# Kernel optimization log

Hardware: AMD Instinct MI355X
Metric: run time of the kernel (lower is better)

## Reference

```python
import jax, jax.numpy as jnp
import numpy as np

N = 100000   # nodes
E = 800000   # edges
IN = 256     # input feature dim
H = 4        # heads per layer
D = 32       # per-head hidden dim (num_hidden)
SLOPE = 0.2  # leaky_relu negative slope


def setup_inputs() -> dict:
    key = jax.random.key(0)
    ks = jax.random.split(key, 8)
    s = 0.1  # weight scale for numerical stability
    x = jax.random.normal(ks[0], (N, IN), jnp.float32)
    edge_index = jax.random.randint(ks[1], (2, E), 0, N, dtype=jnp.int32)
    W0 = jax.random.normal(ks[2], (IN, H * D), jnp.float32) * s
    al0 = jax.random.normal(ks[3], (H, D), jnp.float32) * s
    ar0 = jax.random.normal(ks[4], (H, D), jnp.float32) * s
    W1 = jax.random.normal(ks[5], (H * D, H * D), jnp.float32) * s
    al1 = jax.random.normal(ks[6], (H, D), jnp.float32) * s
    ar1 = jax.random.normal(ks[7], (H, D), jnp.float32) * s
    return {"x": x, "edge_index": edge_index, "W0": W0, "al0": al0,
            "ar0": ar0, "W1": W1, "al1": al1, "ar1": ar1}


def _gat_layer(h, W, al, ar, src, dst, residual):
    """One GATConv: project, edge attention, dst-wise softmax, scatter-agg."""
    n = h.shape[0]
    feat = (h @ W).reshape(n, H, D)              # [N,H,D]
    el = jnp.einsum('nhd,hd->nh', feat, al)      # [N,H]
    er = jnp.einsum('nhd,hd->nh', feat, ar)      # [N,H]
    e = jax.nn.leaky_relu(el[src] + er[dst], SLOPE)   # raw scores [E,H]
    # edge softmax grouped by destination node (numerically stable)
    emax = jax.ops.segment_max(e, dst, num_segments=n)   # [N,H]
    eexp = jnp.exp(e - emax[dst])                          # [E,H]
    denom = jax.ops.segment_sum(eexp, dst, num_segments=n)  # [N,H]
    a = eexp / denom[dst]                                  # attention [E,H]
    msg = feat[src] * a[:, :, None]                        # [E,H,D]
    rst = jax.ops.segment_sum(msg, dst, num_segments=n)    # [N,H,D]
    if residual:
        rst = rst + h.reshape(n, H, D)  # identity residual (dims match)
    rst = jax.nn.elu(rst)               # activation
    return rst, a, e


def reference(x, edge_index, W0, al0, ar0, W1, al1, ar1):
    src, dst = edge_index[0], edge_index[1]
    # layer 0: no residual
    h1, a0, e0 = _gat_layer(x, W0, al0, ar0, src, dst, residual=False)
    atten0 = e0.mean(axis=-1)  # e_gat.flatten(1).mean(-1) -> [E]
    # layer 1: residual
    h2, a1, e1 = _gat_layer(h1.reshape(N, H * D), W1, al1, ar1, src, dst,
                            residual=True)
    atten1 = e1.mean(axis=-1)
    temp = h2.reshape(N, H * D)          # flattened node embeddings
    heads = tuple(h2[:, i] for i in range(H))  # per-head [N,D]
    return (temp,) + heads + (e1, atten0, atten1)
```

## Files before the change

kernel.cpp:

```cpp
#include <hip/hip_runtime.h>
#include <hip/hip_bf16.h>


typedef _Float16 f16;
typedef _Float16 f16x2 __attribute__((ext_vector_type(2)));
typedef _Float16 f16x4 __attribute__((ext_vector_type(4)));
typedef _Float16 f16x8 __attribute__((ext_vector_type(8)));
typedef float f32x2 __attribute__((ext_vector_type(2)));
typedef float f32x4 __attribute__((ext_vector_type(4)));

__device__ __forceinline__ void gload16(const void* g, void* l) {
    __builtin_amdgcn_global_load_lds(
        (const __attribute__((address_space(1))) unsigned int*)g,
        (__attribute__((address_space(3))) unsigned int*)l, 16, 0, 0);
}

__global__ void prep(const float* __restrict__ W0, const float* __restrict__ W1,
                     f16* __restrict__ Wth0, f16* __restrict__ Wtl0,
                     f16* __restrict__ Wth1, f16* __restrict__ Wtl1,
                     const int* __restrict__ dsts, int* __restrict__ deg, int E) {
    int i = blockIdx.x * blockDim.x + threadIdx.x;
    if (i < 256 * 128) {
        int k = i >> 7, c = i & 127;
        float v = W0[i];
        f16 h = (f16)v;
        Wth0[(size_t)c * 256 + k] = h;
        Wtl0[(size_t)c * 256 + k] = (f16)(v - (float)h);
    } else if (i < 256 * 128 + 128 * 128) {
        int j = i - 256 * 128;
        int k = j >> 7, c = j & 127;
        float v = W1[j];
        f16 h = (f16)v;
        Wth1[(size_t)c * 128 + k] = h;
        Wtl1[(size_t)c * 128 + k] = (f16)(v - (float)h);
    } else {
        int e = i - (256 * 128 + 128 * 128);
        if (e < E) atomicAdd(&deg[dsts[e]], 1);
    }
}

template <int AFP16>
__device__ __forceinline__ void gemm_body(
        int bid, const void* __restrict__ Xv, const f16* __restrict__ Wth,
        const f16* __restrict__ Wtl, f16* __restrict__ Y16,
        const float* __restrict__ al, const float* __restrict__ ar,
        float* __restrict__ el_out, float* __restrict__ er_out,
        int nrows, int K) {
    __shared__ float As32[AFP16 ? 1 : 128 * 32];
    __shared__ f16   As16[AFP16 ? 128 * 32 : 1];
    __shared__ f16   Bh[128 * 32];
    __shared__ f16   Bl[128 * 32];
    const int t    = threadIdx.x;
    const int wave = t >> 6;
    const int lane = t & 63;
    const int lr   = lane & 15;
    const int kg   = lane >> 4;
    const int row0 = bid * 128;

    f32x4 acc[2][8];
    #pragma unroll
    for (int i = 0; i < 2; ++i)
        #pragma unroll
        for (int j = 0; j < 8; ++j) acc[i][j] = (f32x4){0.f, 0.f, 0.f, 0.f};

    for (int k0 = 0; k0 < K; k0 += 32) {
        if constexpr (!AFP16) {
            #pragma unroll
            for (int j = 0; j < 4; ++j) {
                int G = t + 256 * j;
                int row = G >> 3, slot = G & 7;
                int g = slot ^ (row & 7);
                int grow = row0 + row; if (grow >= nrows) grow = nrows - 1;
                gload16((const float*)Xv + (size_t)grow * K + k0 + g * 4,
                        &As32[G * 4]);
            }
        } else {
            #pragma unroll
            for (int j = 0; j < 2; ++j) {
                int G = t + 256 * j;
                int row = G >> 2, g4 = G & 3;
                int grow = row0 + row; if (grow >= nrows) grow = nrows - 1;
                gload16((const f16*)Xv + (size_t)grow * K + k0 + g4 * 8,
                        &As16[G * 8]);
            }
        }
        #pragma unroll
        for (int j = 0; j < 2; ++j) {
            int G = t + 256 * j;
            int r = G >> 2, g4 = G & 3;
            int p = ((r & 15) << 3) | (r >> 4);
            gload16(Wth + (size_t)p * K + k0 + g4 * 8, &Bh[G * 8]);
            gload16(Wtl + (size_t)p * K + k0 + g4 * 8, &Bl[G * 8]);
        }
        __syncthreads();

        const int ar0_ = wave * 32 + lr;
        f16x8 ah0, ah1;
        if constexpr (!AFP16) {
            int s0 = (2 * kg) ^ (lr & 7);
            int s1 = (2 * kg + 1) ^ (lr & 7);
            f32x4 u0 = *(const f32x4*)&As32[ar0_ * 32 + s0 * 4];
            f32x4 u1 = *(const f32x4*)&As32[ar0_ * 32 + s1 * 4];
            f32x4 v0 = *(const f32x4*)&As32[(ar0_ + 16) * 32 + s0 * 4];
            f32x4 v1 = *(const f32x4*)&As32[(ar0_ + 16) * 32 + s1 * 4];
            float a8[8] = {u0[0], u0[1], u0[2], u0[3], u1[0], u1[1], u1[2], u1[3]};
            float b8[8] = {v0[0], v0[1], v0[2], v0[3], v1[0], v1[1], v1[2], v1[3]};
            #pragma unroll
            for (int i = 0; i < 8; ++i) {
                ah0[i] = (f16)a8[i];
                ah1[i] = (f16)b8[i];
            }
        } else {
            ah0 = *(const f16x8*)&As16[ar0_ * 32 + kg * 8];
            ah1 = *(const f16x8*)&As16[(ar0_ + 16) * 32 + kg * 8];
        }
        f16x8 bh[8];
        #pragma unroll
        for (int cb = 0; cb < 8; ++cb)
            bh[cb] = *(const f16x8*)&Bh[(cb * 16 + lr) * 32 + kg * 8];

        #pragma unroll
        for (int cb = 0; cb < 8; ++cb) {
            acc[0][cb] = __builtin_amdgcn_mfma_f32_16x16x32_f16(ah0, bh[cb], acc[0][cb], 0, 0, 0);
            acc[1][cb] = __builtin_amdgcn_mfma_f32_16x16x32_f16(ah1, bh[cb], acc[1][cb], 0, 0, 0);
        }
        #pragma unroll
        for (int cb = 0; cb < 8; ++cb) {
            f16x8 bl = *(const f16x8*)&Bl[(cb * 16 + lr) * 32 + kg * 8];
            acc[0][cb] = __builtin_amdgcn_mfma_f32_16x16x32_f16(ah0, bl, acc[0][cb], 0, 0, 0);
            acc[1][cb] = __builtin_amdgcn_mfma_f32_16x16x32_f16(ah1, bl, acc[1][cb], 0, 0, 0);
        }
        __syncthreads();
    }

    const int hh = lr >> 2;
    const int co = (lr & 3) * 8;
    float alv[8], arv[8];
    #pragma unroll
    for (int j = 0; j < 8; ++j) {
        alv[j] = al[hh * 32 + co + j];
        arv[j] = ar[hh * 32 + co + j];
    }
    #pragma unroll
    for (int rb = 0; rb < 2; ++rb) {
        int rbase = row0 + wave * 32 + rb * 16 + kg * 4;
        #pragma unroll
        for (int r = 0; r < 4; ++r) {
            int grow = rbase + r;
            f16x8 hv;
            float sl_ = 0.0f, sr_ = 0.0f;
            #pragma unroll
            for (int cb = 0; cb < 8; ++cb) {
                float v = acc[rb][cb][r];
                hv[cb] = (f16)v;
                sl_ += v * alv[cb];
                sr_ += v * arv[cb];
            }
            sl_ += __shfl_xor(sl_, 1); sl_ += __shfl_xor(sl_, 2);
            sr_ += __shfl_xor(sr_, 1); sr_ += __shfl_xor(sr_, 2);
            if (grow < nrows) {
                *(f16x8*)(Y16 + (size_t)grow * 128 + lr * 8) = hv;
                if ((lane & 3) == 0) {
                    el_out[4 * (size_t)grow + hh] = sl_;
                    er_out[4 * (size_t)grow + hh] = sr_;
                }
            }
        }
    }
}

__device__ __forceinline__ void scan_body(int b, const int* __restrict__ deg,
                                          int* __restrict__ excl,
                                          int* __restrict__ bsums, int n) {
    __shared__ int wsums[4];
    int t = threadIdx.x;
    int base = b * 1024;
    int idx = base + t * 4;
    int v[4];
    #pragma unroll
    for (int i = 0; i < 4; ++i) v[i] = (idx + i < n) ? deg[idx + i] : 0;
    int tsum = v[0] + v[1] + v[2] + v[3];
    int lane = t & 63, wid = t >> 6;
    int incl = tsum;
    #pragma unroll
    for (int off = 1; off < 64; off <<= 1) {
        int u = __shfl_up(incl, off, 64);
        if (lane >= off) incl += u;
    }
    if (lane == 63) wsums[wid] = incl;
    __syncthreads();
    if (t == 0) {
        int s = 0;
        #pragma unroll
        for (int w = 0; w < 4; ++w) { int x = wsums[w]; wsums[w] = s; s += x; }
    }
    __syncthreads();
    int ex = incl - tsum + wsums[wid];
    int run = ex;
    #pragma unroll
    for (int i = 0; i < 4; ++i) { if (idx + i < n) excl[idx + i] = run; run += v[i]; }
    if (t == 255) bsums[b] = ex + tsum;
}

__global__ __launch_bounds__(256, 2) void gemm0_scan(
        const float* __restrict__ X, const f16* __restrict__ Wth,
        const f16* __restrict__ Wtl, f16* __restrict__ Y16,
        const float* __restrict__ al, const float* __restrict__ ar,
        float* __restrict__ el_out, float* __restrict__ er_out,
        int nrows, int K, int gblocks,
        const int* __restrict__ deg, int* __restrict__ excl,
        int* __restrict__ bsums, int n) {
    if ((int)blockIdx.x < gblocks)
        gemm_body<0>(blockIdx.x, X, Wth, Wtl, Y16, al, ar, el_out, er_out, nrows, K);
    else
        scan_body(blockIdx.x - gblocks, deg, excl, bsums, n);
}

__global__ __launch_bounds__(256, 2) void gemm_mfma1(
        const f16* __restrict__ X, const f16* __restrict__ Wth,
        const f16* __restrict__ Wtl, f16* __restrict__ Y16,
        const float* __restrict__ al, const float* __restrict__ ar,
        float* __restrict__ el_out, float* __restrict__ er_out,
        int nrows, int K) {
    gemm_body<1>(blockIdx.x, X, Wth, Wtl, Y16, al, ar, el_out, er_out, nrows, K);
}

__global__ __launch_bounds__(256) void scan_fin(int* __restrict__ row_off,
                                                const int* __restrict__ bsums,
                                                int* __restrict__ cursor,
                                                const int* __restrict__ deg,
                                                int n, int nb) {
    __shared__ int spfx;
    int b = blockIdx.x;
    int t = threadIdx.x;
    if (t < 64) {
        int v = 0;
        if (t < b && t < nb) v = bsums[t];
        int t2 = t + 64;
        if (t2 < b && t2 < nb) v += bsums[t2];
        #pragma unroll
        for (int off = 32; off; off >>= 1) v += __shfl_xor(v, off, 64);
        if (t == 0) spfx = v;
    }
    __syncthreads();
    int pfx = spfx;
    int base = b * 1024 + t * 4;
    #pragma unroll
    for (int i2 = 0; i2 < 4; ++i2) {
        int i = base + i2;
        if (i < n) {
            int v = row_off[i] + pfx;
            row_off[i] = v;
            cursor[i]  = v;
            if (i == n - 1) row_off[n] = v + deg[i];
        }
    }
}

__global__ void fill_csr_edge0(const int* __restrict__ srcs, const int* __restrict__ dsts,
                               int* __restrict__ cursor, int* __restrict__ csr_src,
                               const float* __restrict__ el, const float* __restrict__ er,
                               float* __restrict__ atten0, int E) {
    int e = blockIdx.x * blockDim.x + threadIdx.x;
    if (e >= E) return;
    int s = srcs[e], d = dsts[e];
    int p = atomicAdd(&cursor[d], 1);
    csr_src[p] = s;
    float4 elv = *(const float4*)(el + 4 * (size_t)s);
    float4 erv = *(const float4*)(er + 4 * (size_t)d);
    float v0 = elv.x + erv.x, v1 = elv.y + erv.y;
    float v2 = elv.z + erv.z, v3 = elv.w + erv.w;
    v0 = v0 > 0.0f ? v0 : 0.2f * v0;
    v1 = v1 > 0.0f ? v1 : 0.2f * v1;
    v2 = v2 > 0.0f ? v2 : 0.2f * v2;
    v3 = v3 > 0.0f ? v3 : 0.2f * v3;
    __builtin_nontemporal_store((v0 + v1 + v2 + v3) * 0.25f, atten0 + e);
}

__device__ __forceinline__ void edge1_body(int bid,
        const int* __restrict__ srcs, const int* __restrict__ dsts,
        const float* __restrict__ el, const float* __restrict__ er,
        float* __restrict__ e1_out, float* __restrict__ atten1, int E) {
    int e = bid * 256 + threadIdx.x;
    if (e >= E) return;
    int s = srcs[e], d = dsts[e];
    float4 elv = *(const float4*)(el + 4 * (size_t)s);
    float4 erv = *(const float4*)(er + 4 * (size_t)d);
    float v0 = elv.x + erv.x, v1 = elv.y + erv.y;
    float v2 = elv.z + erv.z, v3 = elv.w + erv.w;
    v0 = v0 > 0.0f ? v0 : 0.2f * v0;
    v1 = v1 > 0.0f ? v1 : 0.2f * v1;
    v2 = v2 > 0.0f ? v2 : 0.2f * v2;
    v3 = v3 > 0.0f ? v3 : 0.2f * v3;
    __builtin_nontemporal_store((f32x4){v0, v1, v2, v3},
                                (f32x4*)(e1_out + 4 * (size_t)e));
    __builtin_nontemporal_store((v0 + v1 + v2 + v3) * 0.25f, atten1 + e);
}

template <int LAYER>
__device__ __forceinline__ void agg_body(int bid,
        const int* __restrict__ row_off, const int* __restrict__ csr_src,
        const float* __restrict__ el, const float* __restrict__ er,
        const f16* __restrict__ feat16, const f16* __restrict__ resid16,
        f16* __restrict__ out16, float* __restrict__ out32,
        float* __restrict__ heads, int N) {
    int wv   = (bid * 256 + (int)threadIdx.x) >> 6;
    int lane = threadIdx.x & 63;
    int half = lane >> 5;
    int node = wv * 2 + half;
    int l31  = lane & 31;
    int q2 = (lane >> 4) & 1;
    int sc = lane & 15;
    int h  = sc >> 2;
    bool valid = node < N;
    int nclamp = valid ? node : N - 1;
    int start = row_off[nclamp];
    int dc    = valid ? (row_off[nclamp + 1] - start) : 0;
    float er_h = er[4 * (size_t)nclamp + h];

    float acc[8];
    #pragma unroll
    for (int j = 0; j < 8; ++j) acc[j] = 0.0f;
    float dh = 0.0f;
    const int base = half << 5;

    for (int cs = 0; cs < dc; cs += 32) {
        int act = dc - cs; if (act > 32) act = 32;
        int sl = (l31 < act) ? csr_src[start + cs + l31] : 0;
        int i = 0;
        for (; i + 4 <= act; i += 4) {
            int s0 = __shfl(sl, base + i + q2);
            int s1 = __shfl(sl, base + i + 2 + q2);
            float x0 = el[4 * (size_t)s0 + h] + er_h;
            float x1 = el[4 * (size_t)s1 + h] + er_h;
            x0 = x0 > 0.0f ? x0 : 0.2f * x0;
            x1 = x1 > 0.0f ? x1 : 0.2f * x1;
            float w0 = __expf(x0);
            float w1 = __expf(x1);
            f16x8 f0 = *(const f16x8*)(feat16 + 128 * (size_t)s0 + sc * 8);
            f16x8 f1 = *(const f16x8*)(feat16 + 128 * (size_t)s1 + sc * 8);
            #pragma unroll
            for (int j = 0; j < 8; ++j) acc[j] += w0 * (float)f0[j];
            #pragma unroll
            for (int j = 0; j < 8; ++j) acc[j] += w1 * (float)f1[j];
            dh += w0 + w1;
        }
        for (; i < act; i += 2) {
            int e = i + q2;
            bool on = e < act;
            int s = __shfl(sl, base + (on ? e : 0));
            float x = el[4 * (size_t)s + h] + er_h;
            x = x > 0.0f ? x : 0.2f * x;
            float w = on ? __expf(x) : 0.0f;
            f16x8 fv = *(const f16x8*)(feat16 + 128 * (size_t)s + sc * 8);
            #pragma unroll
            for (int j = 0; j < 8; ++j) acc[j] += w * (float)fv[j];
            dh += w;
        }
    }

    #pragma unroll
    for (int j = 0; j < 8; ++j) acc[j] += __shfl_xor(acc[j], 16);
    dh += __shfl_xor(dh, 16);
    if (!valid) return;

    float inv = (dc > 0) ? 1.0f / dh : 0.0f;
    float r0 = (q2 ? acc[4] : acc[0]) * inv;
    float r1 = (q2 ? acc[5] : acc[1]) * inv;
    float r2 = (q2 ? acc[6] : acc[2]) * inv;
    float r3 = (q2 ? acc[7] : acc[3]) * inv;
    int c0 = sc * 8 + q2 * 4;
    size_t o = 128 * (size_t)node + c0;
    if (LAYER == 1) {
        f16x4 rv = *(const f16x4*)(resid16 + o);
        r0 += (float)rv[0]; r1 += (float)rv[1];
        r2 += (float)rv[2]; r3 += (float)rv[3];
    }
    r0 = r0 > 0.0f ? r0 : __expf(r0) - 1.0f;
    r1 = r1 > 0.0f ? r1 : __expf(r1) - 1.0f;
    r2 = r2 > 0.0f ? r2 : __expf(r2) - 1.0f;
    r3 = r3 > 0.0f ? r3 : __expf(r3) - 1.0f;
    if (LAYER == 0) {
        f16x4 hv; hv[0] = (f16)r0; hv[1] = (f16)r1; hv[2] = (f16)r2; hv[3] = (f16)r3;
        *(f16x4*)(out16 + o) = hv;
    } else {
        __builtin_nontemporal_store((f32x4){r0, r1, r2, r3}, (f32x4*)(out32 + o));
        __builtin_nontemporal_store(
            (f32x4){r0, r1, r2, r3},
            (f32x4*)(heads + (size_t)h * N * 32 + (size_t)node * 32 + (c0 & 31)));
    }
}

__global__ __launch_bounds__(256) void aggregate0(const int* __restrict__ row_off,
                                                  const int* __restrict__ csr_src,
                                                  const float* __restrict__ el,
                                                  const float* __restrict__ er,
                                                  const f16* __restrict__ feat16,
                                                  f16* __restrict__ out16, int N) {
    agg_body<0>(blockIdx.x, row_off, csr_src, el, er, feat16, nullptr,
                out16, nullptr, nullptr, N);
}

__global__ __launch_bounds__(256) void layer1_fused(
        const int* __restrict__ row_off, const int* __restrict__ csr_src,
        const float* __restrict__ el, const float* __restrict__ er,
        const f16* __restrict__ feat16, const f16* __restrict__ resid16,
        float* __restrict__ out32, float* __restrict__ heads,
        const int* __restrict__ srcs, const int* __restrict__ dsts,
        float* __restrict__ e1_out, float* __restrict__ atten1,
        int aggBlocks, int N, int E) {
    if ((int)blockIdx.x < aggBlocks)
        agg_body<1>(blockIdx.x, row_off, csr_src, el, er, feat16, resid16,
                    nullptr, out32, heads, N);
    else
        edge1_body(blockIdx.x - aggBlocks, srcs, dsts, el, er, e1_out, atten1, E);
}

extern "C" void kernel_launch(void* const* d_in, const int* in_sizes, int n_in,
                              void* d_out, int out_size, void* d_ws, size_t ws_size,
                              hipStream_t stream) {
    const float* x   = (const float*)d_in[0];
    const int*   ei  = (const int*)d_in[1];
    const float* W0  = (const float*)d_in[2];
    const float* al0 = (const float*)d_in[3];
    const float* ar0 = (const float*)d_in[4];
    const float* W1  = (const float*)d_in[5];
    const float* al1 = (const float*)d_in[6];
    const float* ar1 = (const float*)d_in[7];

    const int N = in_sizes[0] / 256;
    const int E = in_sizes[1] / 2;
    const size_t NF = (size_t)N * 128;

    const int* srcs = ei;
    const int* dsts = ei + E;

    float* out = (float*)d_out;
    f16*   f16ws  = (f16*)d_ws;
    f16*   feat16 = f16ws;
    f16*   h1_16  = feat16 + NF;
    float* el   = (float*)(h1_16 + NF);
    float* er   = el + (size_t)N * 4;
    f16*   wth0 = (f16*)(er + (size_t)N * 4);
    f16*   wtl0 = wth0 + (size_t)128 * 256;
    f16*   wth1 = wtl0 + (size_t)128 * 256;
    f16*   wtl1 = wth1 + (size_t)128 * 128;
    int*   ints    = (int*)(wtl1 + (size_t)128 * 128);
    int*   deg     = ints;
    int*   row_off = deg + N;
    int*   cursor  = row_off + N + 1;
    int*   csr_src = cursor + N;
    int*   bsums   = csr_src + E;

    float* heads      = out + NF;
    float* e1_out     = out + 2 * NF;
    float* atten0_out = e1_out + (size_t)E * 4;
    float* atten1_out = atten0_out + E;

    hipMemsetAsync(deg, 0, (size_t)N * sizeof(int), stream);
    const int wtot = 256 * 128 + 128 * 128;
    prep<<<(wtot + E + 255) / 256, 256, 0, stream>>>(W0, W1, wth0, wtl0, wth1, wtl1,
                                                     dsts, deg, E);

    const int gemm_blocks = (N + 127) / 128;
    const int agg_blocks  = (N + 7) / 8;
    const int edge_blocks = (E + 255) / 256;
    const int nb = (N + 1023) / 1024;

    gemm0_scan<<<gemm_blocks + nb, 256, 0, stream>>>(x, wth0, wtl0, feat16, al0, ar0,
                                                     el, er, N, 256, gemm_blocks,
                                                     deg, row_off, bsums, N);
    scan_fin<<<nb, 256, 0, stream>>>(row_off, bsums, cursor, deg, N, nb);
    fill_csr_edge0<<<edge_blocks, 256, 0, stream>>>(srcs, dsts, cursor, csr_src,
                                                    el, er, atten0_out, E);
    aggregate0<<<agg_blocks, 256, 0, stream>>>(row_off, csr_src, el, er,
                                               feat16, h1_16, N);

    gemm_mfma1<<<gemm_blocks, 256, 0, stream>>>(h1_16, wth1, wtl1, feat16, al1, ar1,
                                                el, er, N, 128);
    layer1_fused<<<agg_blocks + edge_blocks, 256, 0, stream>>>(
        row_off, csr_src, el, er, feat16, h1_16, out, heads,
        srcs, dsts, e1_out, atten1_out, agg_blocks, N, E);
}
```

Measured before the change: 406.1 us.

## Drop W1 low-part split, raise GEMM occupancy, unroll aggregation by eight

The layer-1 GEMM now uses only the fp16 high part of W1 and skips the low-part compensation MFMAs and loads, which halves its tensor work and its B-tile LDS traffic. Launch bounds for both GEMM kernels are raised to allow four blocks per CU, which caps register use per thread. The aggregation inner loop gains an eight-edge unrolled path so more gathers are in flight at once. The trade-off is lower precision in the layer-1 projection and possible register spills.

```diff
diff --git a/kernel.cpp b/kernel.cpp
--- a/kernel.cpp
+++ b/kernel.cpp
@@ -17,7 +17,7 @@
 
 __global__ void prep(const float* __restrict__ W0, const float* __restrict__ W1,
                      f16* __restrict__ Wth0, f16* __restrict__ Wtl0,
-                     f16* __restrict__ Wth1, f16* __restrict__ Wtl1,
+                     f16* __restrict__ Wth1,
                      const int* __restrict__ dsts, int* __restrict__ deg, int E) {
     int i = blockIdx.x * blockDim.x + threadIdx.x;
     if (i < 256 * 128) {
@@ -29,10 +29,7 @@
     } else if (i < 256 * 128 + 128 * 128) {
         int j = i - 256 * 128;
         int k = j >> 7, c = j & 127;
-        float v = W1[j];
-        f16 h = (f16)v;
-        Wth1[(size_t)c * 128 + k] = h;
-        Wtl1[(size_t)c * 128 + k] = (f16)(v - (float)h);
+        Wth1[(size_t)c * 128 + k] = (f16)W1[j];
     } else {
         int e = i - (256 * 128 + 128 * 128);
         if (e < E) atomicAdd(&deg[dsts[e]], 1);
@@ -49,7 +46,7 @@
     __shared__ float As32[AFP16 ? 1 : 128 * 32];
     __shared__ f16   As16[AFP16 ? 128 * 32 : 1];
     __shared__ f16   Bh[128 * 32];
-    __shared__ f16   Bl[128 * 32];
+    __shared__ f16   Bl[AFP16 ? 1 : 128 * 32];
     const int t    = threadIdx.x;
     const int wave = t >> 6;
     const int lane = t & 63;
@@ -90,7 +87,8 @@
             int r = G >> 2, g4 = G & 3;
             int p = ((r & 15) << 3) | (r >> 4);
             gload16(Wth + (size_t)p * K + k0 + g4 * 8, &Bh[G * 8]);
-            gload16(Wtl + (size_t)p * K + k0 + g4 * 8, &Bl[G * 8]);
+            if constexpr (!AFP16)
+                gload16(Wtl + (size_t)p * K + k0 + g4 * 8, &Bl[G * 8]);
         }
         __syncthreads();
 
@@ -124,11 +122,13 @@
             acc[0][cb] = __builtin_amdgcn_mfma_f32_16x16x32_f16(ah0, bh[cb], acc[0][cb], 0, 0, 0);
             acc[1][cb] = __builtin_amdgcn_mfma_f32_16x16x32_f16(ah1, bh[cb], acc[1][cb], 0, 0, 0);
         }
-        #pragma unroll
-        for (int cb = 0; cb < 8; ++cb) {
-            f16x8 bl = *(const f16x8*)&Bl[(cb * 16 + lr) * 32 + kg * 8];
-            acc[0][cb] = __builtin_amdgcn_mfma_f32_16x16x32_f16(ah0, bl, acc[0][cb], 0, 0, 0);
-            acc[1][cb] = __builtin_amdgcn_mfma_f32_16x16x32_f16(ah1, bl, acc[1][cb], 0, 0, 0);
+        if constexpr (!AFP16) {
+            #pragma unroll
+            for (int cb = 0; cb < 8; ++cb) {
+                f16x8 bl = *(const f16x8*)&Bl[(cb * 16 + lr) * 32 + kg * 8];
+                acc[0][cb] = __builtin_amdgcn_mfma_f32_16x16x32_f16(ah0, bl, acc[0][cb], 0, 0, 0);
+                acc[1][cb] = __builtin_amdgcn_mfma_f32_16x16x32_f16(ah1, bl, acc[1][cb], 0, 0, 0);
+            }
         }
         __syncthreads();
     }
@@ -202,7 +202,7 @@
     if (t == 255) bsums[b] = ex + tsum;
 }
 
-__global__ __launch_bounds__(256, 2) void gemm0_scan(
+__global__ __launch_bounds__(256, 4) void gemm0_scan(
         const float* __restrict__ X, const f16* __restrict__ Wth,
         const f16* __restrict__ Wtl, f16* __restrict__ Y16,
         const float* __restrict__ al, const float* __restrict__ ar,
@@ -216,13 +216,13 @@
         scan_body(blockIdx.x - gblocks, deg, excl, bsums, n);
 }
 
-__global__ __launch_bounds__(256, 2) void gemm_mfma1(
+__global__ __launch_bounds__(256, 4) void gemm_mfma1(
         const f16* __restrict__ X, const f16* __restrict__ Wth,
-        const f16* __restrict__ Wtl, f16* __restrict__ Y16,
+        f16* __restrict__ Y16,
         const float* __restrict__ al, const float* __restrict__ ar,
         float* __restrict__ el_out, float* __restrict__ er_out,
         int nrows, int K) {
-    gemm_body<1>(blockIdx.x, X, Wth, Wtl, Y16, al, ar, el_out, er_out, nrows, K);
+    gemm_body<1>(blockIdx.x, X, Wth, nullptr, Y16, al, ar, el_out, er_out, nrows, K);
 }
 
 __global__ __launch_bounds__(256) void scan_fin(int* __restrict__ row_off,
@@ -328,6 +328,37 @@
         int act = dc - cs; if (act > 32) act = 32;
         int sl = (l31 < act) ? csr_src[start + cs + l31] : 0;
         int i = 0;
+        for (; i + 8 <= act; i += 8) {
+            int s0 = __shfl(sl, base + i + q2);
+            int s1 = __shfl(sl, base + i + 2 + q2);
+            int s2 = __shfl(sl, base + i + 4 + q2);
+            int s3 = __shfl(sl, base + i + 6 + q2);
+            float x0 = el[4 * (size_t)s0 + h] + er_h;
+            float x1 = el[4 * (size_t)s1 + h] + er_h;
+            float x2 = el[4 * (size_t)s2 + h] + er_h;
+            float x3 = el[4 * (size_t)s3 + h] + er_h;
+            x0 = x0 > 0.0f ? x0 : 0.2f * x0;
+            x1 = x1 > 0.0f ? x1 : 0.2f * x1;
+            x2 = x2 > 0.0f ? x2 : 0.2f * x2;
+            x3 = x3 > 0.0f ? x3 : 0.2f * x3;
+            float w0 = __expf(x0);
+            float w1 = __expf(x1);
+            float w2 = __expf(x2);
+            float w3 = __expf(x3);
+            f16x8 f0 = *(const f16x8*)(feat16 + 128 * (size_t)s0 + sc * 8);
+            f16x8 f1 = *(const f16x8*)(feat16 + 128 * (size_t)s1 + sc * 8);
+            f16x8 f2 = *(const f16x8*)(feat16 + 128 * (size_t)s2 + sc * 8);
+            f16x8 f3 = *(const f16x8*)(feat16 + 128 * (size_t)s3 + sc * 8);
+            #pragma unroll
+            for (int j = 0; j < 8; ++j) acc[j] += w0 * (float)f0[j];
+            #pragma unroll
+            for (int j = 0; j < 8; ++j) acc[j] += w1 * (float)f1[j];
+            #pragma unroll
+            for (int j = 0; j < 8; ++j) acc[j] += w2 * (float)f2[j];
+            #pragma unroll
+            for (int j = 0; j < 8; ++j) acc[j] += w3 * (float)f3[j];
+            dh += w0 + w1 + w2 + w3;
+        }
         for (; i + 4 <= act; i += 4) {
             int s0 = __shfl(sl, base + i + q2);
             int s1 = __shfl(sl, base + i + 2 + q2);
@@ -444,8 +475,7 @@
     f16*   wth0 = (f16*)(er + (size_t)N * 4);
     f16*   wtl0 = wth0 + (size_t)128 * 256;
     f16*   wth1 = wtl0 + (size_t)128 * 256;
-    f16*   wtl1 = wth1 + (size_t)128 * 128;
-    int*   ints    = (int*)(wtl1 + (size_t)128 * 128);
+    int*   ints    = (int*)(wth1 + (size_t)128 * 128);
     int*   deg     = ints;
     int*   row_off = deg + N;
     int*   cursor  = row_off + N + 1;
@@ -459,7 +489,7 @@
 
     hipMemsetAsync(deg, 0, (size_t)N * sizeof(int), stream);
     const int wtot = 256 * 128 + 128 * 128;
-    prep<<<(wtot + E + 255) / 256, 256, 0, stream>>>(W0, W1, wth0, wtl0, wth1, wtl1,
+    prep<<<(wtot + E + 255) / 256, 256, 0, stream>>>(W0, W1, wth0, wtl0, wth1,
                                                      dsts, deg, E);
 
     const int gemm_blocks = (N + 127) / 128;
@@ -476,7 +506,7 @@
     aggregate0<<<agg_blocks, 256, 0, stream>>>(row_off, csr_src, el, er,
                                                feat16, h1_16, N);
 
-    gemm_mfma1<<<gemm_blocks, 256, 0, stream>>>(h1_16, wth1, wtl1, feat16, al1, ar1,
+    gemm_mfma1<<<gemm_blocks, 256, 0, stream>>>(h1_16, wth1, feat16, al1, ar1,
                                                 el, er, N, 128);
     layer1_fused<<<agg_blocks + edge_blocks, 256, 0, stream>>>(
         row_off, csr_src, el, er, feat16, h1_16, out, heads,
```

After: 401.8 us. Within noise of the previous version (-1.1%).
